# Performance work log

Hardware: AMD Instinct MI355X
Metric: run time of the kernel (lower is better)

Reference implementation:

```python
import jax, jax.numpy as jnp
import numpy as np

C = 1.0           # Poincare ball curvature magnitude (k = -1/c with c=1)
MIN_NORM = 1e-15
PROJ_EPS = 4e-3   # geoopt float32 boundary eps


def _artanh(x):
    return jnp.arctanh(jnp.clip(x, -1.0 + 1e-7, 1.0 - 1e-7))


def _norm(x):
    return jnp.maximum(jnp.linalg.norm(x, axis=-1, keepdims=True), MIN_NORM)


def mobius_matvec(W, x, c=C):
    # geoopt pmath.mobius_matvec with k=-c
    sc = jnp.sqrt(c)
    x_norm = _norm(x)
    Mx = x @ W.T
    Mx_norm = _norm(Mx)
    return jnp.tanh(Mx_norm / x_norm * _artanh(sc * x_norm)) * Mx / (Mx_norm * sc)


def mobius_add(x, y, c=C):
    x2 = jnp.sum(x * x, axis=-1, keepdims=True)
    y2 = jnp.sum(y * y, axis=-1, keepdims=True)
    xy = jnp.sum(x * y, axis=-1, keepdims=True)
    num = (1.0 + 2.0 * c * xy + c * y2) * x + (1.0 - c * x2) * y
    den = 1.0 + 2.0 * c * xy + c * c * x2 * y2
    return num / jnp.maximum(den, MIN_NORM)


def project(x, c=C):
    norm = _norm(x)
    maxnorm = (1.0 - PROJ_EPS) / jnp.sqrt(c)
    return jnp.where(norm > maxnorm, x / norm * maxnorm, x)


def expmap0(u, c=C):
    sc = jnp.sqrt(c)
    un = _norm(u)
    return jnp.tanh(sc * un) * u / (sc * un)


def mobius_linear(x, W, b, c=C):
    # hyperbolic_input=True, hyperbolic_bias=True, nonlin=None
    out = mobius_matvec(W, x, c)
    out = mobius_add(out, b, c)
    return project(out, c)


def setup_inputs() -> dict:
    key = jax.random.key(0)
    ks = jax.random.split(key, 7)
    N, D = 2048, 1024        # batch*tlen, input_size
    V = 32000                # output_size (vocab)
    SLEN, B, CV = 512, 32, 500
    hidden = jax.random.normal(ks[0], (N, D), jnp.float32) * 0.1
    hidden = project(hidden)
    attn = jax.random.uniform(ks[1], (N, SLEN), jnp.float32)
    src_map = jax.random.uniform(ks[2], (SLEN, B, CV), jnp.float32)
    W = jax.random.normal(ks[3], (V, D), jnp.float32) * 0.01
    b = expmap0(jax.random.normal(ks[4], (V,), jnp.float32) / 4.0)
    Wc = jax.random.normal(ks[5], (1, D), jnp.float32) * 0.01
    bc = expmap0(jax.random.normal(ks[6], (1,), jnp.float32) / 4.0)
    return {"hidden": hidden, "attn": attn, "src_map": src_map,
            "W": W, "b": b, "Wc": Wc, "bc": bc, "pad_idx": 1}


def reference(hidden, attn, src_map, W, b, Wc, bc, pad_idx):
    slen, batch, cvocab = src_map.shape
    logits = mobius_linear(hidden, W, b)                  # (N, V)
    logits = logits.at[:, pad_idx].set(-jnp.inf)
    prob = jax.nn.softmax(logits, axis=1)
    p_copy = jax.nn.sigmoid(mobius_linear(hidden, Wc, bc))  # (N, 1)
    out_prob = prob * (1.0 - p_copy)
    mul_attn = attn * p_copy                              # (N, slen)
    a = mul_attn.reshape(-1, batch, slen)                 # (tlen, batch, slen)
    copy_prob = jnp.einsum('tbs,sbc->tbc', a, src_map).reshape(-1, cvocab)
    return jnp.concatenate([out_prob, copy_prob], axis=1)
```

## Files before the change

kernel.cpp:

```cpp
#include <hip/hip_runtime.h>
#include <stdint.h>

#define N_ROWS   2048
#define D_IN     1024
#define V_OUT    32000
#define SLEN_C   512
#define BATCH_C  32
#define CVOC     500
#define OUT_COLS 32500

#define MIN_NORM_F 1e-15f
#define PROJ_EPS_F 4e-3f

typedef __bf16 bf16x8_t __attribute__((ext_vector_type(8)));
typedef float  f32x4_t  __attribute__((ext_vector_type(4)));
typedef unsigned short ushort8_t __attribute__((ext_vector_type(8)));

__device__ __forceinline__ unsigned short f2bf(float f) {
    uint32_t b = __float_as_uint(f);
    b += 0x7FFFu + ((b >> 16) & 1u);
    return (unsigned short)(b >> 16);
}
__device__ __forceinline__ float bf2f(unsigned short u) {
    return __uint_as_float(((uint32_t)u) << 16);
}
__device__ __forceinline__ float wave_sum(float v) {
#pragma unroll
    for (int off = 32; off > 0; off >>= 1) v += __shfl_down(v, off, 64);
    return v;
}

__device__ __forceinline__ void load_lds16(const void* g, void* l) {
    __builtin_amdgcn_global_load_lds(
        (const __attribute__((address_space(1))) void*)g,
        (__attribute__((address_space(3))) void*)l, 16, 0, 0);
}

__global__ __launch_bounds__(256)
void cast_f32_to_bf16(const float* __restrict__ src, unsigned short* __restrict__ dst, int n4) {
    int i = blockIdx.x * blockDim.x + threadIdx.x;
    int stride = gridDim.x * blockDim.x;
    for (; i < n4; i += stride) {
        float4 v = ((const float4*)src)[i];
        ushort4 o;
        o.x = f2bf(v.x); o.y = f2bf(v.y); o.z = f2bf(v.z); o.w = f2bf(v.w);
        ((ushort4*)dst)[i] = o;
    }
}

__global__ __launch_bounds__(256)
void row_stats(const float* __restrict__ hidden, const float* __restrict__ Wc,
               const float* __restrict__ bc_in, float* __restrict__ g_arr,
               float* __restrict__ pc_arr) {
    __shared__ float red[8];
    const int n = blockIdx.x;
    const int tid = threadIdx.x;
    float4 hv = *(const float4*)(hidden + (size_t)n * D_IN + tid * 4);
    float4 wv = *(const float4*)(Wc + tid * 4);
    float s = hv.x * hv.x + hv.y * hv.y + hv.z * hv.z + hv.w * hv.w;
    float d = hv.x * wv.x + hv.y * wv.y + hv.z * wv.z + hv.w * wv.w;
    s = wave_sum(s); d = wave_sum(d);
    const int w = tid >> 6, l = tid & 63;
    if (l == 0) { red[w] = s; red[4 + w] = d; }
    __syncthreads();
    if (tid == 0) {
        float S  = red[0] + red[1] + red[2] + red[3];
        float Dc = red[4] + red[5] + red[6] + red[7];
        float xn = fmaxf(sqrtf(S), MIN_NORM_F);
        float xc = fminf(xn, 1.f - 1e-7f);
        float at = 0.5f * logf((1.f + xc) / (1.f - xc));
        float g = at / xn;
        float mxn = fmaxf(fabsf(Dc), MIN_NORM_F);
        float res = tanhf(mxn * g) * (Dc / mxn);
        float bcv = bc_in[0];
        float x2 = res * res, y2 = bcv * bcv, xyv = res * bcv;
        float num = (1.f + 2.f * xyv + y2) * res + (1.f - x2) * bcv;
        float dn  = fmaxf(1.f + 2.f * xyv + x2 * y2, MIN_NORM_F);
        float o = num / dn;
        float an = fmaxf(fabsf(o), MIN_NORM_F);
        float mxp = 1.f - PROJ_EPS_F;
        if (an > mxp) o = o / an * mxp;
        pc_arr[n] = 1.f / (1.f + expf(-o));
        g_arr[n]  = g;
    }
}


#define STG_A(bufi, chunk, kti) \
    load_lds16(Ag + (size_t)(am0 + ((chunk) << 6) + wave8 + srow) * D_IN + ((kti) << 6) + sk, \
               &Asmem[bufi][(((chunk) << 6) + wave8) << 6])
#define STG_B(bufi, chunk, kti) \
    load_lds16(Bg + (size_t)(bn0 + ((chunk) << 6) + wave8 + srow) * D_IN + ((kti) << 6) + sk, \
               &Bsmem[bufi][(((chunk) << 6) + wave8) << 6])

#define VMCNT(N) \
    __builtin_amdgcn_sched_barrier(0); \
    asm volatile("s_waitcnt vmcnt(" #N ")" ::: "memory"); \
    __builtin_amdgcn_sched_barrier(0);

#define RD_A(RB, MH) \
    _Pragma("unroll") for (int i = 0; i < 4; ++i) { \
        const int r_ = (wm + (MH)*64 + i*16 + fr) << 6; \
        af0[i] = *(const bf16x8_t*)&Asmem[RB][r_ + e0]; \
        af1[i] = *(const bf16x8_t*)&Asmem[RB][r_ + e1]; }

#define RD_B(RB, J0) \
    _Pragma("unroll") for (int j = 0; j < 2; ++j) { \
        const int r_ = (wn + ((J0) + j)*16 + fr) << 6; \
        bf0[(J0)+j] = *(const bf16x8_t*)&Bsmem[RB][r_ + e0]; \
        bf1[(J0)+j] = *(const bf16x8_t*)&Bsmem[RB][r_ + e1]; }

#define MM(MH, J0) \
    __builtin_amdgcn_sched_barrier(0); \
    __builtin_amdgcn_s_barrier(); \
    asm volatile("s_waitcnt lgkmcnt(0)" ::: "memory"); \
    __builtin_amdgcn_sched_barrier(0); \
    __builtin_amdgcn_s_setprio(1); \
    _Pragma("unroll") for (int i = 0; i < 4; ++i) \
        _Pragma("unroll") for (int j = 0; j < 2; ++j) { \
            acc[(MH)*4+i][(J0)+j] = __builtin_amdgcn_mfma_f32_16x16x32_bf16(af0[i], bf0[(J0)+j], acc[(MH)*4+i][(J0)+j], 0, 0, 0); \
            acc[(MH)*4+i][(J0)+j] = __builtin_amdgcn_mfma_f32_16x16x32_bf16(af1[i], bf1[(J0)+j], acc[(MH)*4+i][(J0)+j], 0, 0, 0); } \
    __builtin_amdgcn_s_setprio(0); \
    __builtin_amdgcn_s_barrier(); \
    __builtin_amdgcn_sched_barrier(0);

__global__ __launch_bounds__(512, 2)
void gemm_bt_bf16(const unsigned short* __restrict__ Ag,
                  const unsigned short* __restrict__ Bg,
                  unsigned short* __restrict__ Cb)
{
    __shared__ __align__(16) unsigned short Asmem[2][256 * 64];
    __shared__ __align__(16) unsigned short Bsmem[2][256 * 64];
    const int tid  = threadIdx.x;
    const int wave = tid >> 6;
    const int lane = tid & 63;

    const int f   = blockIdx.x;
    const int swz = (f & 7) * 125 + (f >> 3);
    const int am0 = (swz & 7) * 256;
    const int bn0 = (swz >> 3) * 256;

    const int wr = wave >> 2, wc = wave & 3;
    const int wm = wr * 128, wn = wc * 64;
    const int fr  = lane & 15;
    const int fkb = (lane >> 4) << 4;
    const int swzr = (fr & 7) << 4;
    const int e0 = (fkb ^ swzr) >> 1;
    const int e1 = ((64 + fkb) ^ swzr) >> 1;
    const int wave8 = wave << 3;
    const int srow  = lane >> 3;
    const int sk    = ((lane & 7) ^ srow) << 3;

    f32x4_t acc[8][4] = {};
    bf16x8_t af0[4], af1[4], bf0[4], bf1[4];

    STG_A(0, 0, 0); STG_A(0, 2, 0); STG_B(0, 0, 0); STG_B(0, 1, 0);
    STG_B(0, 2, 0); STG_B(0, 3, 0); STG_A(0, 1, 0); STG_A(0, 3, 0);
    STG_A(1, 0, 1); STG_A(1, 2, 1); STG_B(1, 0, 1); STG_B(1, 1, 1);
    STG_B(1, 2, 1); STG_B(1, 3, 1);
    VMCNT(6)
    __builtin_amdgcn_s_barrier();

    for (int t = 0; t < 7; ++t) {
        const int T1 = 2 * t + 1, T2 = 2 * t + 2, T3 = 2 * t + 3;
        RD_A(0, 0); RD_B(0, 0); STG_A(1, 1, T1); STG_A(1, 3, T1); MM(0, 0);
        RD_B(0, 2);             STG_A(0, 0, T2); STG_A(0, 2, T2); MM(0, 2);
        RD_A(0, 1);             STG_B(0, 0, T2); STG_B(0, 1, T2); MM(1, 0);
                                STG_B(0, 2, T2); STG_B(0, 3, T2);
        VMCNT(6)                                                  MM(1, 2);
        RD_A(1, 0); RD_B(1, 0); STG_A(0, 1, T2); STG_A(0, 3, T2); MM(0, 0);
        RD_B(1, 2);             STG_A(1, 0, T3); STG_A(1, 2, T3); MM(0, 2);
        RD_A(1, 1);             STG_B(1, 0, T3); STG_B(1, 1, T3); MM(1, 0);
                                STG_B(1, 2, T3); STG_B(1, 3, T3);
        VMCNT(6)                                                  MM(1, 2);
    }
    RD_A(0, 0); RD_B(0, 0); STG_A(1, 1, 15); STG_A(1, 3, 15); MM(0, 0);
    RD_B(0, 2);                                               MM(0, 2);
    RD_A(0, 1);                                               MM(1, 0);
    VMCNT(0)                                                  MM(1, 2);
    RD_A(1, 0); RD_B(1, 0); MM(0, 0);
    RD_B(1, 2);             MM(0, 2);
    RD_A(1, 1);             MM(1, 0);
                            MM(1, 2);

    unsigned short* slice = (wave < 4) ? (&Asmem[0][0] + (wave << 13))
                                       : (&Bsmem[0][0] + ((wave - 4) << 13));
    const int cm = (lane >> 4) << 2;
    const int cn = lane & 15;
#pragma unroll
    for (int I = 0; I < 8; ++I) {
#pragma unroll
        for (int J = 0; J < 4; ++J) {
#pragma unroll
            for (int r = 0; r < 4; ++r) {
                const int rl  = I * 16 + cm + r;
                const int byt = (rl << 7) + ((J * 16 + cn) << 1);
                *(unsigned short*)((char*)slice + (byt ^ ((rl & 7) << 4))) = f2bf(acc[I][J][r]);
            }
        }
    }
    asm volatile("s_waitcnt lgkmcnt(0)" ::: "memory");
    __builtin_amdgcn_sched_barrier(0);
    const int rl0 = lane >> 3;
    const int bo  = (lane & 7) << 4;
#pragma unroll
    for (int it = 0; it < 16; ++it) {
        const int rl  = rl0 + it * 8;
        const int byt = (rl << 7) + bo;
        uint4 v = *(const uint4*)((const char*)slice + (byt ^ (rl0 << 4)));
        const int mg = am0 + wm + rl;
        char* gp = (char*)Cb + (size_t)mg * (OUT_COLS * 2) + ((size_t)(bn0 + wn) << 1) + bo;
        *(uint2*)gp       = make_uint2(v.x, v.y);
        *(uint2*)(gp + 8) = make_uint2(v.z, v.w);
    }
}

__global__ __launch_bounds__(1024)
void softmax_epi(float* __restrict__ Cout, const float* __restrict__ bvec,
                 const float* __restrict__ g_arr, const float* __restrict__ pc_arr,
                 const int* __restrict__ pad_ptr) {
    __shared__ unsigned short mxls[V_OUT];
    __shared__ float red[48];
    __shared__ float bcast[4];
    const int n = blockIdx.x;
    const int tid = threadIdx.x;
    float* row = Cout + (size_t)n * OUT_COLS;
    const unsigned short* rowb = (const unsigned short*)row;
    const int pad = *pad_ptr;

    float s1 = 0.f, s2 = 0.f, s3 = 0.f;
    for (int i = tid * 8; i < V_OUT; i += 8192) {
        ushort8_t mu = *(const ushort8_t*)(rowb + i);
        float4 b0 = *(const float4*)(bvec + i);
        float4 b1 = *(const float4*)(bvec + i + 4);
        float m0 = bf2f(mu[0]), m1 = bf2f(mu[1]), m2 = bf2f(mu[2]), m3 = bf2f(mu[3]);
        float m4 = bf2f(mu[4]), m5 = bf2f(mu[5]), m6 = bf2f(mu[6]), m7 = bf2f(mu[7]);
        s1 += (m0*m0 + m1*m1 + m2*m2 + m3*m3) + (m4*m4 + m5*m5 + m6*m6 + m7*m7);
        s2 += (m0*b0.x + m1*b0.y + m2*b0.z + m3*b0.w) + (m4*b1.x + m5*b1.y + m6*b1.z + m7*b1.w);
        s3 += (b0.x*b0.x + b0.y*b0.y + b0.z*b0.z + b0.w*b0.w)
            + (b1.x*b1.x + b1.y*b1.y + b1.z*b1.z + b1.w*b1.w);
        *(ushort8_t*)&mxls[i] = mu;
    }
    s1 = wave_sum(s1); s2 = wave_sum(s2); s3 = wave_sum(s3);
    const int w = tid >> 6, l = tid & 63;
    if (l == 0) { red[w] = s1; red[16 + w] = s2; red[32 + w] = s3; }
    __syncthreads();
    if (tid == 0) {
        float S1 = 0.f, S2 = 0.f, Sb = 0.f;
        for (int k = 0; k < 16; ++k) { S1 += red[k]; S2 += red[16 + k]; Sb += red[32 + k]; }
        const float g  = g_arr[n];
        const float r   = fmaxf(sqrtf(S1), MIN_NORM_F);
        const float t   = tanhf(r * g);
        const float smv = t / r;
        const float x2 = smv * smv * S1;
        const float xy = smv * S2;
        const float den = fmaxf(1.f + 2.f * xy + x2 * Sb, MIN_NORM_F);
        float P = (1.f + 2.f * xy + Sb) * smv / den;
        float Q = (1.f - x2) / den;
        const float nrm = fmaxf(sqrtf(P * P * S1 + 2.f * P * Q * S2 + Q * Q * Sb), MIN_NORM_F);
        const float mxp = 1.f - PROJ_EPS_F;
        if (nrm > mxp) { const float fsc = mxp / nrm; P *= fsc; Q *= fsc; }
        bcast[0] = P; bcast[1] = Q;
    }
    __syncthreads();
    const float P = bcast[0], Q = bcast[1];

    float z = 0.f;
    for (int i = tid * 8; i < V_OUT; i += 8192) {
        ushort8_t mu = *(const ushort8_t*)&mxls[i];
        float4 b0 = *(const float4*)(bvec + i);
        float4 b1 = *(const float4*)(bvec + i + 4);
        float e0 = __expf(fmaf(P, bf2f(mu[0]), Q * b0.x));
        float e1 = __expf(fmaf(P, bf2f(mu[1]), Q * b0.y));
        float e2 = __expf(fmaf(P, bf2f(mu[2]), Q * b0.z));
        float e3 = __expf(fmaf(P, bf2f(mu[3]), Q * b0.w));
        float e4 = __expf(fmaf(P, bf2f(mu[4]), Q * b1.x));
        float e5 = __expf(fmaf(P, bf2f(mu[5]), Q * b1.y));
        float e6 = __expf(fmaf(P, bf2f(mu[6]), Q * b1.z));
        float e7 = __expf(fmaf(P, bf2f(mu[7]), Q * b1.w));
        if (i + 0 == pad) e0 = 0.f;
        if (i + 1 == pad) e1 = 0.f;
        if (i + 2 == pad) e2 = 0.f;
        if (i + 3 == pad) e3 = 0.f;
        if (i + 4 == pad) e4 = 0.f;
        if (i + 5 == pad) e5 = 0.f;
        if (i + 6 == pad) e6 = 0.f;
        if (i + 7 == pad) e7 = 0.f;
        z += ((e0 + e1) + (e2 + e3)) + ((e4 + e5) + (e6 + e7));
        ushort8_t eu;
        eu[0] = f2bf(e0); eu[1] = f2bf(e1); eu[2] = f2bf(e2); eu[3] = f2bf(e3);
        eu[4] = f2bf(e4); eu[5] = f2bf(e5); eu[6] = f2bf(e6); eu[7] = f2bf(e7);
        *(ushort8_t*)&mxls[i] = eu;
    }
    z = wave_sum(z);
    if (l == 0) red[w] = z;
    __syncthreads();
    if (tid == 0) {
        float a = 0.f;
        for (int k = 0; k < 16; ++k) a += red[k];
        bcast[2] = a;
    }
    __syncthreads();
    const float scale = (1.f - pc_arr[n]) / bcast[2];

    for (int i = tid * 8; i < V_OUT; i += 8192) {
        ushort8_t eu = *(const ushort8_t*)&mxls[i];
        float4 o0, o1;
        o0.x = bf2f(eu[0]) * scale; o0.y = bf2f(eu[1]) * scale;
        o0.z = bf2f(eu[2]) * scale; o0.w = bf2f(eu[3]) * scale;
        o1.x = bf2f(eu[4]) * scale; o1.y = bf2f(eu[5]) * scale;
        o1.z = bf2f(eu[6]) * scale; o1.w = bf2f(eu[7]) * scale;
        *(float4*)(row + i) = o0;
        *(float4*)(row + i + 4) = o1;
    }
}

__global__ __launch_bounds__(128)
void copy_einsum(const float* __restrict__ attn, const float* __restrict__ src_map,
                 const float* __restrict__ pc_arr, float* __restrict__ Cout) {
    __shared__ float atile[32][128];
    const int tid = threadIdx.x;
    const int cc = blockIdx.x;
    const int b  = blockIdx.y;
    const int t0 = blockIdx.z * 32;
    const int c = cc * 128 + tid;
    const bool cv = (c < CVOC);

    float acc[32];
#pragma unroll
    for (int t = 0; t < 32; ++t) acc[t] = 0.f;

    for (int s0 = 0; s0 < SLEN_C; s0 += 128) {
        __syncthreads();
        for (int idx = tid; idx < 32 * 128; idx += 128) {
            const int t = idx >> 7, s = idx & 127;
            atile[t][s] = attn[(size_t)((t0 + t) * BATCH_C + b) * SLEN_C + s0 + s];
        }
        __syncthreads();
        for (int j = 0; j < 128; j += 4) {
            float sv0 = 0.f, sv1 = 0.f, sv2 = 0.f, sv3 = 0.f;
            if (cv) {
                const float* sp = src_map + (size_t)(s0 + j) * (BATCH_C * CVOC) + b * CVOC + c;
                sv0 = sp[0];
                sv1 = sp[BATCH_C * CVOC];
                sv2 = sp[2 * BATCH_C * CVOC];
                sv3 = sp[3 * BATCH_C * CVOC];
            }
#pragma unroll
            for (int t = 0; t < 32; ++t) {
                const float4 av = *(const float4*)&atile[t][j];
                acc[t] = fmaf(av.x, sv0, acc[t]);
                acc[t] = fmaf(av.y, sv1, acc[t]);
                acc[t] = fmaf(av.z, sv2, acc[t]);
                acc[t] = fmaf(av.w, sv3, acc[t]);
            }
        }
    }
    if (cv) {
#pragma unroll
        for (int t = 0; t < 32; ++t) {
            const int n = (t0 + t) * BATCH_C + b;
            Cout[(size_t)n * OUT_COLS + V_OUT + c] = acc[t] * pc_arr[n];
        }
    }
}

extern "C" void kernel_launch(void* const* d_in, const int* in_sizes, int n_in,
                              void* d_out, int out_size, void* d_ws, size_t ws_size,
                              hipStream_t stream) {
    const float* hidden  = (const float*)d_in[0];
    const float* attn    = (const float*)d_in[1];
    const float* src_map = (const float*)d_in[2];
    const float* W       = (const float*)d_in[3];
    const float* bvec    = (const float*)d_in[4];
    const float* Wc      = (const float*)d_in[5];
    const float* bc      = (const float*)d_in[6];
    const int*   padp    = (const int*)d_in[7];
    float* out = (float*)d_out;

    const int wb_elems = V_OUT * D_IN;
    const int hb_elems = N_ROWS * D_IN;
    unsigned short* Wb = (unsigned short*)d_ws;
    unsigned short* Hb = Wb + wb_elems;
    float* g_arr  = (float*)(Hb + hb_elems);
    float* pc_arr = g_arr + N_ROWS;

    cast_f32_to_bf16<<<4000, 256, 0, stream>>>(W, Wb, wb_elems / 4);
    cast_f32_to_bf16<<<512, 256, 0, stream>>>(hidden, Hb, hb_elems / 4);
    row_stats<<<N_ROWS, 256, 0, stream>>>(hidden, Wc, bc, g_arr, pc_arr);

    gemm_bt_bf16<<<1000, 512, 0, stream>>>(Hb, Wb, (unsigned short*)out);

    softmax_epi<<<N_ROWS, 1024, 0, stream>>>(out, bvec, g_arr, pc_arr, padp);

    dim3 egrid(4, BATCH_C, 2);
    copy_einsum<<<egrid, 128, 0, stream>>>(attn, src_map, pc_arr, out);
}
```

Measured before the change: 727.5 us.

## Merge prep kernels and fold copy einsum into softmax launch

Combines the W cast, hidden cast and row statistics into one prep kernel, with the hidden bf16 cast done inside the row_stats blocks. Appends 128 extra blocks to the softmax epilogue launch that compute the copy einsum, reusing its LDS buffer, with 1024 threads split into quarters over the time dimension. This cuts the launch count from six to three and lets the small einsum overlap with the softmax rows instead of running serially afterwards. The trade-off is register and LDS pressure in the merged kernel and possible tail imbalance from the einsum blocks.

```diff
diff --git a/kernel.cpp b/kernel.cpp
--- a/kernel.cpp
+++ b/kernel.cpp
@@ -37,26 +37,29 @@
 }
 
 __global__ __launch_bounds__(256)
-void cast_f32_to_bf16(const float* __restrict__ src, unsigned short* __restrict__ dst, int n4) {
-    int i = blockIdx.x * blockDim.x + threadIdx.x;
-    int stride = gridDim.x * blockDim.x;
-    for (; i < n4; i += stride) {
-        float4 v = ((const float4*)src)[i];
-        ushort4 o;
-        o.x = f2bf(v.x); o.y = f2bf(v.y); o.z = f2bf(v.z); o.w = f2bf(v.w);
-        ((ushort4*)dst)[i] = o;
-    }
-}
-
-__global__ __launch_bounds__(256)
-void row_stats(const float* __restrict__ hidden, const float* __restrict__ Wc,
-               const float* __restrict__ bc_in, float* __restrict__ g_arr,
-               float* __restrict__ pc_arr) {
+void prep(const float* __restrict__ W, unsigned short* __restrict__ Wb,
+          const float* __restrict__ hidden, unsigned short* __restrict__ Hb,
+          const float* __restrict__ Wc, const float* __restrict__ bc_in,
+          float* __restrict__ g_arr, float* __restrict__ pc_arr) {
+    const int tid = threadIdx.x;
+    if (blockIdx.x < 4000) {
+        const int n4 = V_OUT * D_IN / 4;
+        int i = blockIdx.x * 256 + tid;
+        for (; i < n4; i += 4000 * 256) {
+            float4 v = ((const float4*)W)[i];
+            ushort4 o;
+            o.x = f2bf(v.x); o.y = f2bf(v.y); o.z = f2bf(v.z); o.w = f2bf(v.w);
+            ((ushort4*)Wb)[i] = o;
+        }
+        return;
+    }
     __shared__ float red[8];
-    const int n = blockIdx.x;
-    const int tid = threadIdx.x;
+    const int n = blockIdx.x - 4000;
     float4 hv = *(const float4*)(hidden + (size_t)n * D_IN + tid * 4);
     float4 wv = *(const float4*)(Wc + tid * 4);
+    ushort4 h4;
+    h4.x = f2bf(hv.x); h4.y = f2bf(hv.y); h4.z = f2bf(hv.z); h4.w = f2bf(hv.w);
+    ((ushort4*)(Hb + (size_t)n * D_IN))[tid] = h4;
     float s = hv.x * hv.x + hv.y * hv.y + hv.z * hv.z + hv.w * hv.w;
     float d = hv.x * wv.x + hv.y * wv.y + hv.z * wv.z + hv.w * wv.w;
     s = wave_sum(s); d = wave_sum(d);
@@ -216,14 +219,66 @@
 }
 
 __global__ __launch_bounds__(1024)
-void softmax_epi(float* __restrict__ Cout, const float* __restrict__ bvec,
-                 const float* __restrict__ g_arr, const float* __restrict__ pc_arr,
-                 const int* __restrict__ pad_ptr) {
-    __shared__ unsigned short mxls[V_OUT];
+void softmax_copy(float* __restrict__ Cout, const float* __restrict__ bvec,
+                  const float* __restrict__ g_arr, const float* __restrict__ pc_arr,
+                  const int* __restrict__ pad_ptr,
+                  const float* __restrict__ attn, const float* __restrict__ src_map) {
+    __shared__ __align__(16) unsigned short mxls[V_OUT];
     __shared__ float red[48];
     __shared__ float bcast[4];
+    const int tid = threadIdx.x;
+
+    if (blockIdx.x >= N_ROWS) {
+        const int bidx  = blockIdx.x - N_ROWS;
+        const int b     = bidx & 31;
+        const int t0    = ((bidx >> 5) & 1) * 32;
+        const int chalf = bidx >> 6;
+        const int c     = chalf * 256 + (tid & 255);
+        const int quart = tid >> 8;
+        const bool cv   = (c < CVOC);
+        float (*atile)[128] = reinterpret_cast<float(*)[128]>(mxls);
+
+        float acc[8];
+#pragma unroll
+        for (int tt = 0; tt < 8; ++tt) acc[tt] = 0.f;
+
+        for (int s0 = 0; s0 < SLEN_C; s0 += 128) {
+            __syncthreads();
+            for (int idx = tid; idx < 32 * 128; idx += 1024) {
+                const int t = idx >> 7, s = idx & 127;
+                atile[t][s] = attn[(size_t)((t0 + t) * BATCH_C + b) * SLEN_C + s0 + s];
+            }
+            __syncthreads();
+            for (int j = 0; j < 128; j += 4) {
+                float sv0 = 0.f, sv1 = 0.f, sv2 = 0.f, sv3 = 0.f;
+                if (cv) {
+                    const float* sp = src_map + (size_t)(s0 + j) * (BATCH_C * CVOC) + b * CVOC + c;
+                    sv0 = sp[0];
+                    sv1 = sp[BATCH_C * CVOC];
+                    sv2 = sp[2 * BATCH_C * CVOC];
+                    sv3 = sp[3 * BATCH_C * CVOC];
+                }
+#pragma unroll
+                for (int tt = 0; tt < 8; ++tt) {
+                    const float4 av = *(const float4*)&atile[quart * 8 + tt][j];
+                    acc[tt] = fmaf(av.x, sv0, acc[tt]);
+                    acc[tt] = fmaf(av.y, sv1, acc[tt]);
+                    acc[tt] = fmaf(av.z, sv2, acc[tt]);
+                    acc[tt] = fmaf(av.w, sv3, acc[tt]);
+                }
+            }
+        }
+        if (cv) {
+#pragma unroll
+            for (int tt = 0; tt < 8; ++tt) {
+                const int n = (t0 + quart * 8 + tt) * BATCH_C + b;
+                Cout[(size_t)n * OUT_COLS + V_OUT + c] = acc[tt] * pc_arr[n];
+            }
+        }
+        return;
+    }
+
     const int n = blockIdx.x;
-    const int tid = threadIdx.x;
     float* row = Cout + (size_t)n * OUT_COLS;
     const unsigned short* rowb = (const unsigned short*)row;
     const int pad = *pad_ptr;
@@ -315,56 +370,6 @@
     }
 }
 
-__global__ __launch_bounds__(128)
-void copy_einsum(const float* __restrict__ attn, const float* __restrict__ src_map,
-                 const float* __restrict__ pc_arr, float* __restrict__ Cout) {
-    __shared__ float atile[32][128];
-    const int tid = threadIdx.x;
-    const int cc = blockIdx.x;
-    const int b  = blockIdx.y;
-    const int t0 = blockIdx.z * 32;
-    const int c = cc * 128 + tid;
-    const bool cv = (c < CVOC);
-
-    float acc[32];
-#pragma unroll
-    for (int t = 0; t < 32; ++t) acc[t] = 0.f;
-
-    for (int s0 = 0; s0 < SLEN_C; s0 += 128) {
-        __syncthreads();
-        for (int idx = tid; idx < 32 * 128; idx += 128) {
-            const int t = idx >> 7, s = idx & 127;
-            atile[t][s] = attn[(size_t)((t0 + t) * BATCH_C + b) * SLEN_C + s0 + s];
-        }
-        __syncthreads();
-        for (int j = 0; j < 128; j += 4) {
-            float sv0 = 0.f, sv1 = 0.f, sv2 = 0.f, sv3 = 0.f;
-            if (cv) {
-                const float* sp = src_map + (size_t)(s0 + j) * (BATCH_C * CVOC) + b * CVOC + c;
-                sv0 = sp[0];
-                sv1 = sp[BATCH_C * CVOC];
-                sv2 = sp[2 * BATCH_C * CVOC];
-                sv3 = sp[3 * BATCH_C * CVOC];
-            }
-#pragma unroll
-            for (int t = 0; t < 32; ++t) {
-                const float4 av = *(const float4*)&atile[t][j];
-                acc[t] = fmaf(av.x, sv0, acc[t]);
-                acc[t] = fmaf(av.y, sv1, acc[t]);
-                acc[t] = fmaf(av.z, sv2, acc[t]);
-                acc[t] = fmaf(av.w, sv3, acc[t]);
-            }
-        }
-    }
-    if (cv) {
-#pragma unroll
-        for (int t = 0; t < 32; ++t) {
-            const int n = (t0 + t) * BATCH_C + b;
-            Cout[(size_t)n * OUT_COLS + V_OUT + c] = acc[t] * pc_arr[n];
-        }
-    }
-}
-
 extern "C" void kernel_launch(void* const* d_in, const int* in_sizes, int n_in,
                               void* d_out, int out_size, void* d_ws, size_t ws_size,
                               hipStream_t stream) {
@@ -385,14 +390,10 @@
     float* g_arr  = (float*)(Hb + hb_elems);
     float* pc_arr = g_arr + N_ROWS;
 
-    cast_f32_to_bf16<<<4000, 256, 0, stream>>>(W, Wb, wb_elems / 4);
-    cast_f32_to_bf16<<<512, 256, 0, stream>>>(hidden, Hb, hb_elems / 4);
-    row_stats<<<N_ROWS, 256, 0, stream>>>(hidden, Wc, bc, g_arr, pc_arr);
+    prep<<<4000 + N_ROWS, 256, 0, stream>>>(W, Wb, hidden, Hb, Wc, bc, g_arr, pc_arr);
 
     gemm_bt_bf16<<<1000, 512, 0, stream>>>(Hb, Wb, (unsigned short*)out);
 
-    softmax_epi<<<N_ROWS, 1024, 0, stream>>>(out, bvec, g_arr, pc_arr, padp);
-
-    dim3 egrid(4, BATCH_C, 2);
-    copy_einsum<<<egrid, 128, 0, stream>>>(attn, src_map, pc_arr, out);
-}
+    softmax_copy<<<N_ROWS + 128, 1024, 0, stream>>>(out, bvec, g_arr, pc_arr, padp,
+                                                    attn, src_map);
+}
```

Result: slower. 1.103 ms (+51.6%).
